# Optimization experiments

Hardware: AMD Instinct MI355X
Metric: run time of the kernel (lower is better)

## Reference

```python
import jax, jax.numpy as jnp
import numpy as np

LOG2 = float(np.log(2.0))

def ssp(x):
    # shifted softplus used by SchNet
    return jax.nn.softplus(x) - LOG2

def setup_inputs() -> dict:
    key = jax.random.key(0)
    k1, k2, k3, k4, k5 = jax.random.split(key, 5)
    N, E, D, F = 100000, 600000, 128, 64
    nodes = jax.random.normal(k1, (N, D), dtype=jnp.float32)
    edges = jax.random.normal(k2, (E, F), dtype=jnp.float32)
    edges_i = jax.random.randint(k3, (E, 2), 0, N, dtype=jnp.int64)
    W1 = jax.random.normal(k4, (F, D), dtype=jnp.float32) * (1.0 / np.sqrt(F))
    b1 = jnp.zeros((D,), dtype=jnp.float32)
    W2 = jax.random.normal(k5, (D, D), dtype=jnp.float32) * (1.0 / np.sqrt(D))
    b2 = jnp.zeros((D,), dtype=jnp.float32)
    return {"nodes": nodes, "edges": edges, "edges_i": edges_i,
            "W1": W1, "b1": b1, "W2": W2, "b2": b2}

def reference(nodes, edges, edges_i, W1, b1, W2, b2):
    starts = edges_i[:, 0]  # [E]
    ends = edges_i[:, 1]    # [E]
    # edge MLP filter: two Dense layers with shifted-softplus
    filt = ssp(edges @ W1 + b1)   # [E, D]
    filt = ssp(filt @ W2 + b2)    # [E, D]
    # gather end nodes, modulate by filter, scatter-add onto start nodes
    msgs = nodes[ends] * filt     # [E, D]
    return nodes.at[starts].add(msgs)  # [N, D]
```

## Files before the change

kernel.cpp:

```cpp
#include <hip/hip_runtime.h>
#include <math.h>

#define DD 128
#define FF 64
#define BM 64
#define SENT 0xFFFFFFFFu

typedef __attribute__((ext_vector_type(8))) short bf16x8;
typedef __attribute__((ext_vector_type(4))) short short4s;
typedef __attribute__((ext_vector_type(4))) float f32x4;

__device__ __forceinline__ float ssp_f(float x) {
    float ax = fabsf(x);
    float e  = __expf(-ax);
    return fmaxf(x, 0.0f) + __logf(1.0f + e) - 0.6931471805599453f;
}

__device__ __forceinline__ unsigned short f2bf(float f) {
    unsigned u = __float_as_uint(f);
    unsigned r = (u + 0x7FFFu + ((u >> 16) & 1u)) >> 16;
    return (unsigned short)r;
}
__device__ __forceinline__ float bf2f(unsigned short h) {
    return __uint_as_float(((unsigned)h) << 16);
}

__global__ void copy_nodes_kernel(const float4* __restrict__ src,
                                  float4* __restrict__ dst, int n4) {
    int i = blockIdx.x * blockDim.x + threadIdx.x;
    int stride = gridDim.x * blockDim.x;
    for (; i < n4; i += stride) dst[i] = src[i];
}

__global__ void zero_u32_kernel(unsigned* __restrict__ p, int n) {
    int i = blockIdx.x * blockDim.x + threadIdx.x;
    int stride = gridDim.x * blockDim.x;
    for (; i < n; i += stride) p[i] = 0u;
}

__global__ void hist_kernel(const int* __restrict__ eidx,
                            unsigned* __restrict__ counts, int E) {
    int e = blockIdx.x * blockDim.x + threadIdx.x;
    if (e < E) atomicAdd(&counts[eidx[2 * e]], 1u);
}

__global__ void scan1_kernel(const unsigned* __restrict__ counts,
                             unsigned* __restrict__ cursor,
                             unsigned* __restrict__ bsums, int n) {
    __shared__ unsigned s[256];
    int i = blockIdx.x * 256 + threadIdx.x;
    unsigned v = (i < n) ? counts[i] : 0u;
    s[threadIdx.x] = v;
    __syncthreads();
    #pragma unroll
    for (int d = 1; d < 256; d <<= 1) {
        unsigned t = (threadIdx.x >= d) ? s[threadIdx.x - d] : 0u;
        __syncthreads();
        s[threadIdx.x] += t;
        __syncthreads();
    }
    if (i < n) cursor[i] = s[threadIdx.x] - v;
    if (threadIdx.x == 255) bsums[blockIdx.x] = s[255];
}

__global__ void scan2_kernel(unsigned* __restrict__ bsums, int nb) {
    __shared__ unsigned s[512];
    int t = threadIdx.x;
    if (nb <= 512) {
        unsigned v = (t < nb) ? bsums[t] : 0u;
        s[t] = v;
        __syncthreads();
        #pragma unroll
        for (int d = 1; d < 512; d <<= 1) {
            unsigned x = (t >= d) ? s[t - d] : 0u;
            __syncthreads();
            s[t] += x;
            __syncthreads();
        }
        if (t < nb) bsums[t] = s[t] - v;
    } else if (t == 0) {
        unsigned run = 0u;
        for (int i = 0; i < nb; ++i) { unsigned x = bsums[i]; bsums[i] = run; run += x; }
    }
}

__global__ void scan3_kernel(unsigned* __restrict__ cursor,
                             const unsigned* __restrict__ bsums, int n) {
    int i = blockIdx.x * 256 + threadIdx.x;
    if (i < n) cursor[i] += bsums[blockIdx.x];
}

__global__ void scatter_ids_kernel(const int* __restrict__ eidx,
                                   unsigned* __restrict__ cursor,
                                   unsigned* __restrict__ sorted_e,
                                   unsigned* __restrict__ sorted_nt,
                                   unsigned* __restrict__ sorted_ns, int E) {
    int e = blockIdx.x * blockDim.x + threadIdx.x;
    if (e < E) {
        int ns = eidx[2 * e];
        unsigned pos = atomicAdd(&cursor[ns], 1u);
        sorted_e[pos]  = (unsigned)e;
        sorted_nt[pos] = (unsigned)eidx[2 * e + 1];
        sorted_ns[pos] = (unsigned)ns;
    }
}

__global__ void prep_w_kernel(const float* __restrict__ W, int K,
                              unsigned short* __restrict__ hi,
                              unsigned short* __restrict__ lo) {
    int S = K >> 5;
    int idx = blockIdx.x * blockDim.x + threadIdx.x;
    int total = 8 * S * 64;
    if (idx >= total) return;
    int l = idx & 63;
    int s = (idx >> 6) % S;
    int j = idx / (64 * S);
    int col = j * 16 + (l & 15);
    int kbase = s * 32 + (l >> 4) * 8;
    int ob = ((j * S + s) * 64 + l) * 8;
    #pragma unroll
    for (int i = 0; i < 8; ++i) {
        float w = W[(size_t)(kbase + i) * DD + col];
        unsigned short h = f2bf(w);
        hi[ob + i] = h;
        lo[ob + i] = f2bf(w - bf2f(h));
    }
}

__launch_bounds__(256, 4)
__global__ void edge_mfma_kernel(const float* __restrict__ nodes,
                                 const float* __restrict__ edges,
                                 const unsigned* __restrict__ sorted_e,
                                 const unsigned* __restrict__ sorted_nt,
                                 const unsigned* __restrict__ sorted_ns,
                                 const unsigned* __restrict__ ends,
                                 const unsigned short* __restrict__ W1h,
                                 const unsigned short* __restrict__ W1l,
                                 const unsigned short* __restrict__ W2h,
                                 const unsigned short* __restrict__ W2l,
                                 const float* __restrict__ b1,
                                 const float* __restrict__ b2,
                                 float* __restrict__ out,
                                 float* __restrict__ bpart,
                                 unsigned* __restrict__ bnode,
                                 int E) {
    __shared__ unsigned short smem[BM * DD * 2];
    unsigned short* aHi = smem;
    unsigned short* aLo = smem + BM * FF;
    unsigned short* fHi = smem;
    unsigned short* fLo = smem + BM * DD;
    float* SM = reinterpret_cast<float*>(smem);

    const int t = threadIdx.x;
    const int tile = blockIdx.x;
    const int tlo = tile * BM;

    unsigned ns_reg = (tlo + (t & 63) < E) ? sorted_ns[tlo + (t & 63)] : SENT;

    const float4* e4 = reinterpret_cast<const float4*>(edges);
    #pragma unroll
    for (int it = 0; it < 4; ++it) {
        int idx = it * 256 + t;
        int row = idx >> 4, c4 = idx & 15;
        int i = tlo + row;
        float4 v = make_float4(0.f, 0.f, 0.f, 0.f);
        if (i < E) {
            unsigned e = sorted_e[i];
            v = e4[(size_t)e * (FF / 4) + c4];
        }
        unsigned short h0 = f2bf(v.x), h1 = f2bf(v.y), h2 = f2bf(v.z), h3 = f2bf(v.w);
        short4s hv = { (short)h0, (short)h1, (short)h2, (short)h3 };
        short4s lv = { (short)f2bf(v.x - bf2f(h0)), (short)f2bf(v.y - bf2f(h1)),
                       (short)f2bf(v.z - bf2f(h2)), (short)f2bf(v.w - bf2f(h3)) };
        int g = c4 >> 1, half = c4 & 1;
        int off = row * FF + ((g ^ (row & 7)) * 8) + half * 4;
        *reinterpret_cast<short4s*>(aHi + off) = hv;
        *reinterpret_cast<short4s*>(aLo + off) = lv;
    }
    __syncthreads();

    const int lane = t & 63, wave = t >> 6;
    const int wrow = wave * 16;
    const int lr = lane & 15, lg = lane >> 4;

    bf16x8 a1h[2], a1l[2];
    #pragma unroll
    for (int s = 0; s < 2; ++s) {
        int row = wrow + lr;
        int g = s * 4 + lg;
        int off = row * FF + ((g ^ (row & 7)) * 8);
        a1h[s] = *reinterpret_cast<const bf16x8*>(aHi + off);
        a1l[s] = *reinterpret_cast<const bf16x8*>(aLo + off);
    }
    __syncthreads();

    f32x4 zero4 = { 0.f, 0.f, 0.f, 0.f };
    f32x4 acc1[8];
    #pragma unroll
    for (int j = 0; j < 8; ++j) acc1[j] = zero4;
    #pragma unroll
    for (int j = 0; j < 8; ++j) {
        bf16x8 bh[2], bl[2];
        #pragma unroll
        for (int s = 0; s < 2; ++s) {
            bh[s] = *reinterpret_cast<const bf16x8*>(W1h + ((size_t)((j * 2 + s) * 64 + lane)) * 8);
            bl[s] = *reinterpret_cast<const bf16x8*>(W1l + ((size_t)((j * 2 + s) * 64 + lane)) * 8);
        }
        #pragma unroll
        for (int s = 0; s < 2; ++s) {
            acc1[j] = __builtin_amdgcn_mfma_f32_16x16x32_bf16(a1h[s], bh[s], acc1[j], 0, 0, 0);
            acc1[j] = __builtin_amdgcn_mfma_f32_16x16x32_bf16(a1h[s], bl[s], acc1[j], 0, 0, 0);
            acc1[j] = __builtin_amdgcn_mfma_f32_16x16x32_bf16(a1l[s], bh[s], acc1[j], 0, 0, 0);
        }
    }

    #pragma unroll
    for (int j = 0; j < 8; ++j) {
        int col = j * 16 + lr;
        float bv = b1[col];
        #pragma unroll
        for (int r = 0; r < 4; ++r) {
            int row = wrow + lg * 4 + r;
            float f = ssp_f(acc1[j][r] + bv);
            unsigned short h = f2bf(f);
            unsigned short l2 = f2bf(f - bf2f(h));
            int off = row * DD + (((col >> 3) ^ (row & 7)) * 8) + (col & 7);
            fHi[off] = h;
            fLo[off] = l2;
        }
    }
    __syncthreads();

    bf16x8 a2h[4], a2l[4];
    #pragma unroll
    for (int s = 0; s < 4; ++s) {
        int row = wrow + lr;
        int g = s * 4 + lg;
        int off = row * DD + ((g ^ (row & 7)) * 8);
        a2h[s] = *reinterpret_cast<const bf16x8*>(fHi + off);
        a2l[s] = *reinterpret_cast<const bf16x8*>(fLo + off);
    }
    __syncthreads();

    f32x4 acc2[8];
    #pragma unroll
    for (int j = 0; j < 8; ++j) acc2[j] = zero4;
    #pragma unroll
    for (int j = 0; j < 8; ++j) {
        bf16x8 bh[4], bl[4];
        #pragma unroll
        for (int s = 0; s < 4; ++s) {
            bh[s] = *reinterpret_cast<const bf16x8*>(W2h + ((size_t)((j * 4 + s) * 64 + lane)) * 8);
            bl[s] = *reinterpret_cast<const bf16x8*>(W2l + ((size_t)((j * 4 + s) * 64 + lane)) * 8);
        }
        #pragma unroll
        for (int s = 0; s < 4; ++s) {
            acc2[j] = __builtin_amdgcn_mfma_f32_16x16x32_bf16(a2h[s], bh[s], acc2[j], 0, 0, 0);
            acc2[j] = __builtin_amdgcn_mfma_f32_16x16x32_bf16(a2h[s], bl[s], acc2[j], 0, 0, 0);
            acc2[j] = __builtin_amdgcn_mfma_f32_16x16x32_bf16(a2l[s], bh[s], acc2[j], 0, 0, 0);
        }
    }

    #pragma unroll
    for (int j = 0; j < 8; ++j) {
        int col = j * 16 + lr;
        float bv = b2[col];
        #pragma unroll
        for (int r = 0; r < 4; ++r) {
            int row = wrow + lg * 4 + r;
            SM[row * DD + (col ^ ((row & 7) << 2))] = ssp_f(acc2[j][r] + bv);
        }
    }
    __syncthreads();

    #pragma unroll
    for (int it = 0; it < 8; ++it) {
        int idx = it * 256 + t;
        int row = idx >> 5, c4 = idx & 31;
        unsigned nt = (tlo + row < E) ? sorted_nt[tlo + row] : 0u;
        float4 nv = reinterpret_cast<const float4*>(nodes)[(size_t)nt * 32 + c4];
        int foff = row * DD + ((c4 * 4) ^ ((row & 7) << 2));
        float4 mv = *reinterpret_cast<float4*>(SM + foff);
        mv.x *= nv.x; mv.y *= nv.y; mv.z *= nv.z; mv.w *= nv.w;
        *reinterpret_cast<float4*>(SM + foff) = mv;
    }
    __syncthreads();

    if (t < DD) {
        const int col = t;
        unsigned n0 = __shfl(ns_reg, 0);
        unsigned s0 = (n0 == 0u) ? 0u : ends[n0 - 1];
        bool contFirst = (s0 < (unsigned)tlo);
        if (t == 0) bnode[tile] = contFirst ? n0 : SENT;

        float acc = 0.f;
        unsigned cur = n0;
        int segstart = 0;
        #pragma unroll 1
        for (int r = 0; r < BM; ++r) {
            unsigned n = __shfl(ns_reg, r);
            if (n != cur) {
                if (segstart == 0 && contFirst)
                    bpart[(size_t)tile * DD + col] = acc;
                else
                    out[(size_t)cur * DD + col] = nodes[(size_t)cur * DD + col] + acc;
                cur = n; acc = 0.f; segstart = r;
            }
            acc += SM[r * DD + (col ^ ((r & 7) << 2))];
        }
        if (cur != SENT) {
            if (segstart == 0 && contFirst)
                bpart[(size_t)tile * DD + col] = acc;
            else
                out[(size_t)cur * DD + col] = nodes[(size_t)cur * DD + col] + acc;
        }
    }
}

__global__ void fixup_bpart_kernel(const float* __restrict__ bpart,
                                   const unsigned* __restrict__ bnode,
                                   float* __restrict__ out, int NT) {
    int ti = blockIdx.x * 2 + (threadIdx.x >> 7);
    if (ti >= NT) return;
    unsigned n = bnode[ti];
    if (n == SENT) return;
    int c = threadIdx.x & 127;
    atomicAdd(&out[(size_t)n * DD + c], bpart[(size_t)ti * DD + c]);
}

__global__ void copy_empty_kernel(const unsigned* __restrict__ counts,
                                  const float4* __restrict__ nodes4,
                                  float4* __restrict__ out4, int N) {
    int n = blockIdx.x * 8 + (threadIdx.x >> 5);
    if (n >= N) return;
    if (counts[n] != 0u) return;
    int d4 = threadIdx.x & 31;
    out4[(size_t)n * 32 + d4] = nodes4[(size_t)n * 32 + d4];
}

__launch_bounds__(256, 2)
__global__ void edge_fused_atomic_kernel(const float* __restrict__ nodes,
                                         const float* __restrict__ edges,
                                         const int*   __restrict__ eidx,
                                         const float* __restrict__ W1,
                                         const float* __restrict__ b1,
                                         const float* __restrict__ W2,
                                         const float* __restrict__ b2,
                                         float* __restrict__ out, int E) {
    int e = blockIdx.x * 256 + threadIdx.x;
    if (e >= E) return;
    int ns = eidx[2 * e + 0];
    int nt = eidx[2 * e + 1];

    float h1[DD];
    #pragma unroll
    for (int d = 0; d < DD; ++d) h1[d] = b1[d];
    const float4* ev4 = reinterpret_cast<const float4*>(edges) + (size_t)e * (FF / 4);
    #pragma unroll 1
    for (int f4 = 0; f4 < FF / 4; ++f4) {
        float4 ev = ev4[f4];
        const float* w0 = W1 + (size_t)(f4 * 4) * DD;
        #pragma unroll
        for (int d = 0; d < DD; ++d) h1[d] = fmaf(ev.x, w0[d], h1[d]);
        #pragma unroll
        for (int d = 0; d < DD; ++d) h1[d] = fmaf(ev.y, w0[DD + d], h1[d]);
        #pragma unroll
        for (int d = 0; d < DD; ++d) h1[d] = fmaf(ev.z, w0[2 * DD + d], h1[d]);
        #pragma unroll
        for (int d = 0; d < DD; ++d) h1[d] = fmaf(ev.w, w0[3 * DD + d], h1[d]);
    }
    #pragma unroll
    for (int d = 0; d < DD; ++d) h1[d] = ssp_f(h1[d]);

    const float* nrow = nodes + (size_t)nt * DD;
    float*       orow = out   + (size_t)ns * DD;
    #pragma unroll 1
    for (int c = 0; c < 2; ++c) {
        const int base = c * 64;
        float h2[64];
        #pragma unroll
        for (int j = 0; j < 64; ++j) h2[j] = b2[base + j];
        #pragma unroll
        for (int k = 0; k < DD; ++k) {
            float hk = h1[k];
            const float* w = W2 + (size_t)k * DD + base;
            #pragma unroll
            for (int j = 0; j < 64; ++j) h2[j] = fmaf(hk, w[j], h2[j]);
        }
        #pragma unroll
        for (int j = 0; j < 64; ++j) {
            float m = ssp_f(h2[j]) * nrow[base + j];
            __hip_atomic_fetch_add(&orow[base + j], m,
                                   __ATOMIC_RELAXED, __HIP_MEMORY_SCOPE_AGENT);
        }
    }
}

extern "C" void kernel_launch(void* const* d_in, const int* in_sizes, int n_in,
                              void* d_out, int out_size, void* d_ws, size_t ws_size,
                              hipStream_t stream) {
    const float* nodes = (const float*)d_in[0];
    const float* edges = (const float*)d_in[1];
    const int*   eidx  = (const int*)  d_in[2];
    const float* W1    = (const float*)d_in[3];
    const float* b1    = (const float*)d_in[4];
    const float* W2    = (const float*)d_in[5];
    const float* b2    = (const float*)d_in[6];
    float* out = (float*)d_out;

    int ND = in_sizes[0];
    int N  = ND / DD;
    int E  = in_sizes[1] / FF;
    int NT = (E + BM - 1) / BM;

    int nb = (N + 255) / 256;
    uintptr_t base = (uintptr_t)d_ws;
    uintptr_t p = base;
    unsigned* counts    = (unsigned*)p;  p += (size_t)N * 4;
    unsigned* cursor    = (unsigned*)p;  p += (size_t)N * 4;
    unsigned* bsums     = (unsigned*)p;  p += (size_t)nb * 4;
    unsigned* sorted_e  = (unsigned*)p;  p += (size_t)E * 4;
    unsigned* sorted_nt = (unsigned*)p;  p += (size_t)E * 4;
    unsigned* sorted_ns = (unsigned*)p;  p += (size_t)E * 4;
    p = (p + 255) & ~(uintptr_t)255;
    unsigned short* W1h = (unsigned short*)p;  p += (size_t)FF * DD * 2;
    unsigned short* W1l = (unsigned short*)p;  p += (size_t)FF * DD * 2;
    unsigned short* W2h = (unsigned short*)p;  p += (size_t)DD * DD * 2;
    unsigned short* W2l = (unsigned short*)p;  p += (size_t)DD * DD * 2;
    unsigned* bnode     = (unsigned*)p;  p += (size_t)NT * 4;
    p = (p + 255) & ~(uintptr_t)255;
    float* bpart        = (float*)p;     p += (size_t)NT * DD * 4;

    if ((size_t)(p - base) > ws_size) {
        copy_nodes_kernel<<<dim3(1024), dim3(256), 0, stream>>>(
            (const float4*)nodes, (float4*)out, ND / 4);
        edge_fused_atomic_kernel<<<dim3((E + 255) / 256), dim3(256), 0, stream>>>(
            nodes, edges, eidx, W1, b1, W2, b2, out, E);
        return;
    }

    prep_w_kernel<<<dim3(4), dim3(256), 0, stream>>>(W1, FF, W1h, W1l);
    prep_w_kernel<<<dim3(8), dim3(256), 0, stream>>>(W2, DD, W2h, W2l);

    zero_u32_kernel<<<dim3(256), dim3(256), 0, stream>>>(counts, N);
    hist_kernel<<<dim3((E + 255) / 256), dim3(256), 0, stream>>>(eidx, counts, E);
    scan1_kernel<<<dim3(nb), dim3(256), 0, stream>>>(counts, cursor, bsums, N);
    scan2_kernel<<<dim3(1), dim3(512), 0, stream>>>(bsums, nb);
    scan3_kernel<<<dim3(nb), dim3(256), 0, stream>>>(cursor, bsums, N);
    scatter_ids_kernel<<<dim3((E + 255) / 256), dim3(256), 0, stream>>>(
        eidx, cursor, sorted_e, sorted_nt, sorted_ns, E);

    copy_empty_kernel<<<dim3((N + 7) / 8), dim3(256), 0, stream>>>(
        counts, (const float4*)nodes, (float4*)out, N);

    edge_mfma_kernel<<<dim3(NT), dim3(256), 0, stream>>>(
        nodes, edges, sorted_e, sorted_nt, sorted_ns, cursor,
        W1h, W1l, W2h, W2l, b1, b2, out, bpart, bnode, E);

    fixup_bpart_kernel<<<dim3((NT + 1) / 2), dim3(256), 0, stream>>>(
        bpart, bnode, out, NT);
}
```

Measured before the change: 448.5 us.

## Persistent 128-edge tiles with LDS-resident weights, prefetch, and reduced split-bf16 MFMA

Turns the edge MLP kernel into a persistent grid of 512-thread blocks that each loop over 128-edge tiles. The hi/lo bf16 weights are staged once into LDS rather than read from global memory per tile, and the next tile's edge features are prefetched into registers. Activations now use a single bf16 term, dropping the lo-activation MFMA pass (two MFMAs per step instead of three) at some cost in precision. The scatter stage is split into two 64-column halves to fit the smaller LDS region, which adds barriers and leaves occupancy limited by the large LDS footprint.

```diff
diff --git a/kernel.cpp b/kernel.cpp
--- a/kernel.cpp
+++ b/kernel.cpp
@@ -3,7 +3,7 @@
 
 #define DD 128
 #define FF 64
-#define BM 64
+#define BM2 128
 #define SENT 0xFFFFFFFFu
 
 typedef __attribute__((ext_vector_type(8))) short bf16x8;
@@ -127,7 +127,7 @@
     }
 }
 
-__launch_bounds__(256, 4)
+__launch_bounds__(512, 2)
 __global__ void edge_mfma_kernel(const float* __restrict__ nodes,
                                  const float* __restrict__ edges,
                                  const unsigned* __restrict__ sorted_e,
@@ -143,176 +143,206 @@
                                  float* __restrict__ out,
                                  float* __restrict__ bpart,
                                  unsigned* __restrict__ bnode,
-                                 int E) {
-    __shared__ unsigned short smem[BM * DD * 2];
-    unsigned short* aHi = smem;
-    unsigned short* aLo = smem + BM * FF;
-    unsigned short* fHi = smem;
-    unsigned short* fLo = smem + BM * DD;
-    float* SM = reinterpret_cast<float*>(smem);
+                                 int NT, int E) {
+    __shared__ unsigned short w1hS[8192];
+    __shared__ unsigned short w1lS[8192];
+    __shared__ unsigned short w2hS[16384];
+    __shared__ unsigned short w2lS[16384];
+    __shared__ unsigned short region[16384];
+    float* SM = reinterpret_cast<float*>(region);
 
     const int t = threadIdx.x;
-    const int tile = blockIdx.x;
-    const int tlo = tile * BM;
-
-    unsigned ns_reg = (tlo + (t & 63) < E) ? sorted_ns[tlo + (t & 63)] : SENT;
-
-    const float4* e4 = reinterpret_cast<const float4*>(edges);
-    #pragma unroll
-    for (int it = 0; it < 4; ++it) {
-        int idx = it * 256 + t;
-        int row = idx >> 4, c4 = idx & 15;
-        int i = tlo + row;
-        float4 v = make_float4(0.f, 0.f, 0.f, 0.f);
-        if (i < E) {
-            unsigned e = sorted_e[i];
-            v = e4[(size_t)e * (FF / 4) + c4];
-        }
-        unsigned short h0 = f2bf(v.x), h1 = f2bf(v.y), h2 = f2bf(v.z), h3 = f2bf(v.w);
-        short4s hv = { (short)h0, (short)h1, (short)h2, (short)h3 };
-        short4s lv = { (short)f2bf(v.x - bf2f(h0)), (short)f2bf(v.y - bf2f(h1)),
-                       (short)f2bf(v.z - bf2f(h2)), (short)f2bf(v.w - bf2f(h3)) };
-        int g = c4 >> 1, half = c4 & 1;
-        int off = row * FF + ((g ^ (row & 7)) * 8) + half * 4;
-        *reinterpret_cast<short4s*>(aHi + off) = hv;
-        *reinterpret_cast<short4s*>(aLo + off) = lv;
-    }
-    __syncthreads();
-
     const int lane = t & 63, wave = t >> 6;
     const int wrow = wave * 16;
     const int lr = lane & 15, lg = lane >> 4;
-
-    bf16x8 a1h[2], a1l[2];
-    #pragma unroll
-    for (int s = 0; s < 2; ++s) {
-        int row = wrow + lr;
-        int g = s * 4 + lg;
-        int off = row * FF + ((g ^ (row & 7)) * 8);
-        a1h[s] = *reinterpret_cast<const bf16x8*>(aHi + off);
-        a1l[s] = *reinterpret_cast<const bf16x8*>(aLo + off);
+    const int arow = t >> 2, aqc = t & 3;
+
+    #pragma unroll
+    for (int i = 0; i < 2; ++i) {
+        int k = i * 512 + t;
+        reinterpret_cast<bf16x8*>(w1hS)[k] = reinterpret_cast<const bf16x8*>(W1h)[k];
+        reinterpret_cast<bf16x8*>(w1lS)[k] = reinterpret_cast<const bf16x8*>(W1l)[k];
+    }
+    #pragma unroll
+    for (int i = 0; i < 4; ++i) {
+        int k = i * 512 + t;
+        reinterpret_cast<bf16x8*>(w2hS)[k] = reinterpret_cast<const bf16x8*>(W2h)[k];
+        reinterpret_cast<bf16x8*>(w2lS)[k] = reinterpret_cast<const bf16x8*>(W2l)[k];
+    }
+
+    const float4* e4 = reinterpret_cast<const float4*>(edges);
+    const f32x4 zero4 = { 0.f, 0.f, 0.f, 0.f };
+
+    float4 pfv[4];
+    {
+        int rn = blockIdx.x * BM2 + arow;
+        unsigned seN = (rn < E) ? sorted_e[rn] : SENT;
+        #pragma unroll
+        for (int c = 0; c < 4; ++c)
+            pfv[c] = (seN != SENT) ? e4[(size_t)seN * 16 + aqc * 4 + c]
+                                   : make_float4(0.f, 0.f, 0.f, 0.f);
     }
     __syncthreads();
 
-    f32x4 zero4 = { 0.f, 0.f, 0.f, 0.f };
-    f32x4 acc1[8];
-    #pragma unroll
-    for (int j = 0; j < 8; ++j) acc1[j] = zero4;
-    #pragma unroll
-    for (int j = 0; j < 8; ++j) {
-        bf16x8 bh[2], bl[2];
+    for (int tp = blockIdx.x; tp < NT; tp += gridDim.x) {
+        const int tlo = tp * BM2;
+
+        #pragma unroll
+        for (int c = 0; c < 4; ++c) {
+            int c4 = aqc * 4 + c;
+            int g = c4 >> 1, half = c4 & 1;
+            short4s hv = { (short)f2bf(pfv[c].x), (short)f2bf(pfv[c].y),
+                           (short)f2bf(pfv[c].z), (short)f2bf(pfv[c].w) };
+            *reinterpret_cast<short4s*>(region + arow * 64 +
+                ((g ^ (arow & 7)) * 8 + half * 4)) = hv;
+        }
+        __syncthreads();
+
+        {
+            int tn = tp + (int)gridDim.x;
+            unsigned seN = SENT;
+            if (tn < NT) {
+                int rn = tn * BM2 + arow;
+                if (rn < E) seN = sorted_e[rn];
+            }
+            #pragma unroll
+            for (int c = 0; c < 4; ++c)
+                pfv[c] = (seN != SENT) ? e4[(size_t)seN * 16 + aqc * 4 + c]
+                                       : make_float4(0.f, 0.f, 0.f, 0.f);
+        }
+
+        bf16x8 a1[2];
         #pragma unroll
         for (int s = 0; s < 2; ++s) {
-            bh[s] = *reinterpret_cast<const bf16x8*>(W1h + ((size_t)((j * 2 + s) * 64 + lane)) * 8);
-            bl[s] = *reinterpret_cast<const bf16x8*>(W1l + ((size_t)((j * 2 + s) * 64 + lane)) * 8);
-        }
-        #pragma unroll
-        for (int s = 0; s < 2; ++s) {
-            acc1[j] = __builtin_amdgcn_mfma_f32_16x16x32_bf16(a1h[s], bh[s], acc1[j], 0, 0, 0);
-            acc1[j] = __builtin_amdgcn_mfma_f32_16x16x32_bf16(a1h[s], bl[s], acc1[j], 0, 0, 0);
-            acc1[j] = __builtin_amdgcn_mfma_f32_16x16x32_bf16(a1l[s], bh[s], acc1[j], 0, 0, 0);
-        }
-    }
-
-    #pragma unroll
-    for (int j = 0; j < 8; ++j) {
-        int col = j * 16 + lr;
-        float bv = b1[col];
-        #pragma unroll
-        for (int r = 0; r < 4; ++r) {
-            int row = wrow + lg * 4 + r;
-            float f = ssp_f(acc1[j][r] + bv);
-            unsigned short h = f2bf(f);
-            unsigned short l2 = f2bf(f - bf2f(h));
-            int off = row * DD + (((col >> 3) ^ (row & 7)) * 8) + (col & 7);
-            fHi[off] = h;
-            fLo[off] = l2;
-        }
-    }
-    __syncthreads();
-
-    bf16x8 a2h[4], a2l[4];
-    #pragma unroll
-    for (int s = 0; s < 4; ++s) {
-        int row = wrow + lr;
-        int g = s * 4 + lg;
-        int off = row * DD + ((g ^ (row & 7)) * 8);
-        a2h[s] = *reinterpret_cast<const bf16x8*>(fHi + off);
-        a2l[s] = *reinterpret_cast<const bf16x8*>(fLo + off);
-    }
-    __syncthreads();
-
-    f32x4 acc2[8];
-    #pragma unroll
-    for (int j = 0; j < 8; ++j) acc2[j] = zero4;
-    #pragma unroll
-    for (int j = 0; j < 8; ++j) {
-        bf16x8 bh[4], bl[4];
+            int row = wrow + lr;
+            int g = s * 4 + lg;
+            a1[s] = *reinterpret_cast<const bf16x8*>(region + row * 64 + ((g ^ (row & 7)) * 8));
+        }
+
+        f32x4 acc1[8];
+        #pragma unroll
+        for (int j = 0; j < 8; ++j) acc1[j] = zero4;
+        #pragma unroll
+        for (int j = 0; j < 8; ++j) {
+            #pragma unroll
+            for (int s = 0; s < 2; ++s) {
+                bf16x8 wh = *reinterpret_cast<const bf16x8*>(w1hS + ((j * 2 + s) * 64 + lane) * 8);
+                bf16x8 wl = *reinterpret_cast<const bf16x8*>(w1lS + ((j * 2 + s) * 64 + lane) * 8);
+                acc1[j] = __builtin_amdgcn_mfma_f32_16x16x32_bf16(a1[s], wh, acc1[j], 0, 0, 0);
+                acc1[j] = __builtin_amdgcn_mfma_f32_16x16x32_bf16(a1[s], wl, acc1[j], 0, 0, 0);
+            }
+        }
+        __syncthreads();
+
+        #pragma unroll
+        for (int j = 0; j < 8; ++j) {
+            int col = j * 16 + lr;
+            float bv = b1[col];
+            int gc = col >> 3, ci = col & 7;
+            #pragma unroll
+            for (int r = 0; r < 4; ++r) {
+                int row = wrow + lg * 4 + r;
+                region[row * 128 + ((gc ^ (row & 15)) * 8 + ci)] =
+                    f2bf(ssp_f(acc1[j][r] + bv));
+            }
+        }
+        __syncthreads();
+
+        bf16x8 a2[4];
         #pragma unroll
         for (int s = 0; s < 4; ++s) {
-            bh[s] = *reinterpret_cast<const bf16x8*>(W2h + ((size_t)((j * 4 + s) * 64 + lane)) * 8);
-            bl[s] = *reinterpret_cast<const bf16x8*>(W2l + ((size_t)((j * 4 + s) * 64 + lane)) * 8);
-        }
-        #pragma unroll
-        for (int s = 0; s < 4; ++s) {
-            acc2[j] = __builtin_amdgcn_mfma_f32_16x16x32_bf16(a2h[s], bh[s], acc2[j], 0, 0, 0);
-            acc2[j] = __builtin_amdgcn_mfma_f32_16x16x32_bf16(a2h[s], bl[s], acc2[j], 0, 0, 0);
-            acc2[j] = __builtin_amdgcn_mfma_f32_16x16x32_bf16(a2l[s], bh[s], acc2[j], 0, 0, 0);
-        }
-    }
-
-    #pragma unroll
-    for (int j = 0; j < 8; ++j) {
-        int col = j * 16 + lr;
-        float bv = b2[col];
-        #pragma unroll
-        for (int r = 0; r < 4; ++r) {
-            int row = wrow + lg * 4 + r;
-            SM[row * DD + (col ^ ((row & 7) << 2))] = ssp_f(acc2[j][r] + bv);
-        }
-    }
-    __syncthreads();
-
-    #pragma unroll
-    for (int it = 0; it < 8; ++it) {
-        int idx = it * 256 + t;
-        int row = idx >> 5, c4 = idx & 31;
-        unsigned nt = (tlo + row < E) ? sorted_nt[tlo + row] : 0u;
-        float4 nv = reinterpret_cast<const float4*>(nodes)[(size_t)nt * 32 + c4];
-        int foff = row * DD + ((c4 * 4) ^ ((row & 7) << 2));
-        float4 mv = *reinterpret_cast<float4*>(SM + foff);
-        mv.x *= nv.x; mv.y *= nv.y; mv.z *= nv.z; mv.w *= nv.w;
-        *reinterpret_cast<float4*>(SM + foff) = mv;
-    }
-    __syncthreads();
-
-    if (t < DD) {
-        const int col = t;
-        unsigned n0 = __shfl(ns_reg, 0);
-        unsigned s0 = (n0 == 0u) ? 0u : ends[n0 - 1];
-        bool contFirst = (s0 < (unsigned)tlo);
-        if (t == 0) bnode[tile] = contFirst ? n0 : SENT;
-
-        float acc = 0.f;
-        unsigned cur = n0;
-        int segstart = 0;
-        #pragma unroll 1
-        for (int r = 0; r < BM; ++r) {
-            unsigned n = __shfl(ns_reg, r);
-            if (n != cur) {
-                if (segstart == 0 && contFirst)
-                    bpart[(size_t)tile * DD + col] = acc;
-                else
-                    out[(size_t)cur * DD + col] = nodes[(size_t)cur * DD + col] + acc;
-                cur = n; acc = 0.f; segstart = r;
-            }
-            acc += SM[r * DD + (col ^ ((r & 7) << 2))];
-        }
-        if (cur != SENT) {
-            if (segstart == 0 && contFirst)
-                bpart[(size_t)tile * DD + col] = acc;
-            else
-                out[(size_t)cur * DD + col] = nodes[(size_t)cur * DD + col] + acc;
+            int row = wrow + lr;
+            int g = s * 4 + lg;
+            a2[s] = *reinterpret_cast<const bf16x8*>(region + row * 128 + ((g ^ (row & 15)) * 8));
+        }
+        __syncthreads();
+
+        float4 nv[8];
+        #pragma unroll
+        for (int it = 0; it < 8; ++it) {
+            int idx = it * 512 + t;
+            int row = idx >> 5, c4 = idx & 31;
+            unsigned nt_ = (tlo + row < E) ? sorted_nt[tlo + row] : 0u;
+            nv[it] = reinterpret_cast<const float4*>(nodes)[(size_t)nt_ * 32 + c4];
+        }
+
+        f32x4 acc2[8];
+        #pragma unroll
+        for (int j = 0; j < 8; ++j) acc2[j] = zero4;
+        #pragma unroll
+        for (int j = 0; j < 8; ++j) {
+            #pragma unroll
+            for (int s = 0; s < 4; ++s) {
+                bf16x8 wh = *reinterpret_cast<const bf16x8*>(w2hS + ((j * 4 + s) * 64 + lane) * 8);
+                bf16x8 wl = *reinterpret_cast<const bf16x8*>(w2lS + ((j * 4 + s) * 64 + lane) * 8);
+                acc2[j] = __builtin_amdgcn_mfma_f32_16x16x32_bf16(a2[s], wh, acc2[j], 0, 0, 0);
+                acc2[j] = __builtin_amdgcn_mfma_f32_16x16x32_bf16(a2[s], wl, acc2[j], 0, 0, 0);
+            }
+        }
+
+        unsigned nsa = (tlo + lane < E) ? sorted_ns[tlo + lane] : SENT;
+        unsigned nsb = (tlo + 64 + lane < E) ? sorted_ns[tlo + 64 + lane] : SENT;
+
+        #pragma unroll
+        for (int h = 0; h < 2; ++h) {
+            #pragma unroll
+            for (int jj = 0; jj < 4; ++jj) {
+                int j = h * 4 + jj;
+                int col = j * 16 + lr;
+                float bv = b2[col];
+                int colh = col - h * 64;
+                #pragma unroll
+                for (int r = 0; r < 4; ++r) {
+                    int row = wrow + lg * 4 + r;
+                    SM[row * 64 + (colh ^ (((row >> 2) & 3) << 4))] =
+                        ssp_f(acc2[j][r] + bv);
+                }
+            }
+            __syncthreads();
+
+            if (((t & 31) >> 4) == h) {
+                int c4h = t & 15;
+                #pragma unroll
+                for (int it = 0; it < 8; ++it) {
+                    int row = it * 16 + (t >> 5);
+                    int off = row * 64 + ((c4h * 4) ^ (((row >> 2) & 3) << 4));
+                    float4 m = *reinterpret_cast<float4*>(SM + off);
+                    m.x *= nv[it].x; m.y *= nv[it].y; m.z *= nv[it].z; m.w *= nv[it].w;
+                    *reinterpret_cast<float4*>(SM + off) = m;
+                }
+            }
+            __syncthreads();
+
+            if (t < 64) {
+                int col = h * 64 + t;
+                unsigned n0 = __shfl(nsa, 0);
+                unsigned s0 = (n0 == 0u) ? 0u : ends[n0 - 1];
+                bool contFirst = (s0 < (unsigned)tlo);
+                if (t == 0 && h == 0) bnode[tp] = contFirst ? n0 : SENT;
+
+                float acc = 0.f;
+                unsigned cur = n0;
+                int segstart = 0;
+                #pragma unroll 1
+                for (int r = 0; r < BM2; ++r) {
+                    unsigned n = (r < 64) ? __shfl(nsa, r) : __shfl(nsb, r - 64);
+                    if (n != cur) {
+                        if (segstart == 0 && contFirst)
+                            bpart[(size_t)tp * DD + col] = acc;
+                        else
+                            out[(size_t)cur * DD + col] = nodes[(size_t)cur * DD + col] + acc;
+                        cur = n; acc = 0.f; segstart = r;
+                    }
+                    acc += SM[r * 64 + (t ^ (((r >> 2) & 3) << 4))];
+                }
+                if (cur != SENT) {
+                    if (segstart == 0 && contFirst)
+                        bpart[(size_t)tp * DD + col] = acc;
+                    else
+                        out[(size_t)cur * DD + col] = nodes[(size_t)cur * DD + col] + acc;
+                }
+            }
+            __syncthreads();
         }
     }
 }
@@ -411,7 +441,7 @@
     int ND = in_sizes[0];
     int N  = ND / DD;
     int E  = in_sizes[1] / FF;
-    int NT = (E + BM - 1) / BM;
+    int NT = (E + BM2 - 1) / BM2;
 
     int nb = (N + 255) / 256;
     uintptr_t base = (uintptr_t)d_ws;
@@ -453,9 +483,10 @@
     copy_empty_kernel<<<dim3((N + 7) / 8), dim3(256), 0, stream>>>(
         counts, (const float4*)nodes, (float4*)out, N);
 
-    edge_mfma_kernel<<<dim3(NT), dim3(256), 0, stream>>>(
+    int G = (NT < 512) ? NT : 512;
+    edge_mfma_kernel<<<dim3(G), dim3(512), 0, stream>>>(
         nodes, edges, sorted_e, sorted_nt, sorted_ns, cursor,
-        W1h, W1l, W2h, W2l, b1, b2, out, bpart, bnode, E);
+        W1h, W1l, W2h, W2l, b1, b2, out, bpart, bnode, NT, E);
 
     fixup_bpart_kernel<<<dim3((NT + 1) / 2), dim3(256), 0, stream>>>(
         bpart, bnode, out, NT);
```

New measurement: 1.063 ms. +137.1%, slower.
